# Kernel tuning notes

Measured on AMD Instinct MI355X. Metric: run time of the kernel, lower is better.

The kernel has to match this reference:

```python
import jax, jax.numpy as jnp
import numpy as np
from jax import lax


def _sobel_kernels3d(n1=1, n2=2, n3=2):
    Sx = np.asarray([[[-n1, 0, n1], [-n2, 0, n2], [-n1, 0, n1]],
                     [[-n2, 0, n2], [-n3 * n2, 0, n3 * n2], [-n2, 0, n2]],
                     [[-n1, 0, n1], [-n2, 0, n2], [-n1, 0, n1]]])
    Sy = np.asarray([[[-n1, -n2, -n1], [0, 0, 0], [n1, n2, n1]],
                     [[-n2, -n3 * n2, -n2], [0, 0, 0], [n2, n3 * n2, n2]],
                     [[-n1, -n2, -n1], [0, 0, 0], [n1, n2, n1]]])
    Sz = np.asarray([[[-n1, -n2, -n1], [-n2, -n3 * n2, -n2], [-n1, -n2, -n1]],
                     [[0, 0, 0], [0, 0, 0], [0, 0, 0]],
                     [[n1, n2, n1], [n2, n3 * n2, n2], [n1, n2, n1]]])
    Sd11 = np.asarray([[[0, n1, n2], [-n1, 0, n1], [-n2, -n1, 0]],
                       [[0, n2, n2 * n3], [-n2, 0, n2], [-n2 * n3, -n2, 0]],
                       [[0, n1, n2], [-n1, 0, n1], [-n2, -n1, 0]]])
    Sd12 = np.asarray([[[-n2, -n1, 0], [-n1, 0, n1], [0, n1, n2]],
                       [[-n2 * n3, -n2, 0], [-n2, 0, n2], [0, n2, n2 * n3]],
                       [[-n2, -n1, 0], [-n1, 0, n1], [0, n1, n2]]])
    Sd21 = Sd11.T
    Sd22 = Sd12.T
    Sd31 = np.asarray([-S.T for S in Sd11.T])
    Sd32 = np.asarray([S.T for S in Sd12.T])
    S = [Sx, Sy, Sz, Sd11, Sd12, Sd21, Sd22, Sd31, Sd32]
    # (9, 1, 3, 3, 3) OIDHW conv weight bank
    return np.stack(S).astype(np.float32)[:, None]


def _grad_edge3d(img, kernels, a=1):
    # img: (B, C, H, W, D); kernels: (9, 1, 3, 3, 3)
    B, C, H, W, D = img.shape
    p = jnp.pad(img, ((0, 0), (0, 0), (a, a), (a, a), (a, a)), mode='reflect')
    Hp, Wp, Dp = H + 2 * a, W + 2 * a, D + 2 * a
    # Each channel convolved independently with all 9 kernels in one conv call.
    xin = p.reshape(B * C, 1, Hp, Wp, Dp)
    conv = lax.conv_general_dilated(
        xin, kernels, window_strides=(1, 1, 1), padding='SAME',
        dimension_numbers=('NCDHW', 'OIDHW', 'NCDHW'))  # (B*C, 9, Hp, Wp, Dp)
    conv = conv.reshape(B, C, 9, Hp, Wp, Dp)
    # torch: sum_c (conv + 1e-6), squared per-filter, then sum_s (. + 1e-6), sqrt, * 1/C
    per_filter = jnp.sum(conv + 1e-6, axis=1)           # (B, 9, Hp, Wp, Dp)
    mag = jnp.sqrt(jnp.sum(per_filter ** 2, axis=1) + 9 * 1e-6) / C  # (B, Hp, Wp, Dp)
    mag = mag[:, a:-a, a:-a, a:-a]                      # (B, H, W, D)
    mn = mag.min()
    mx = mag.max()
    norm = (mag - mn) / (mx - mn + 1e-6)
    return norm.reshape(B, 1, H, W, D)


def setup_inputs() -> dict:
    key = jax.random.key(0)
    kx, ky = jax.random.split(key)
    B, C, H, W, D = 4, 1, 128, 128, 128
    x = jax.random.normal(kx, (B, C, H, W, D), dtype=jnp.float32)
    y = jax.random.normal(ky, (B, C, H, W, D), dtype=jnp.float32)
    kernels = jnp.asarray(_sobel_kernels3d(1, 2, 2))
    return {"x": x, "y": y, "kernels": kernels}


def reference(x, y, kernels):
    edge_x = _grad_edge3d(x, kernels)
    edge_y = _grad_edge3d(y, kernels)
    # lam_errors = [(1.0, L1Loss())], reduction='sum' -> 1e-6 + 1.0 * mean|ex-ey|
    l1 = jnp.mean(jnp.abs(edge_x - edge_y))
    return 1e-6 + 1.0 * l1
```

## Files before the change

kernel.cpp:

```cpp
#include <hip/hip_runtime.h>
#include <hip/hip_fp16.h>

#define HH 128
#define NB 4
#define NVOX (NB * HH * HH * HH)

#define NBLK1 2048
#define GRID2 512
#define TPB 256

typedef float vf2 __attribute__((ext_vector_type(2)));

__device__ __align__(16) unsigned int g_bmin[NBLK1];
__device__ __align__(16) unsigned int g_bmax[NBLK1];

union U4H8 { uint4 u; __half2 h[4]; };

__global__ __launch_bounds__(256) void pass1_kernel(
    const float* __restrict__ x, const float* __restrict__ y,
    __half* __restrict__ magx, __half* __restrict__ magy,
    float* __restrict__ out) {
    int bid = blockIdx.x;
    int tid = threadIdx.x;
    if (bid == 0 && tid == 0) out[0] = 0.0f;

    int lane = tid & 63, wid = tid >> 6;
    int wg  = bid & 15;
    int hs  = (bid >> 4) & 15;
    int b   = (bid >> 8) & 3;
    int img = bid >> 10;

    const float* __restrict__ src = img ? y : x;
    __half* __restrict__ dst = img ? magy : magx;

    int w0 = wg * 8 + wid * 2;
    int w1 = w0 + 1;
    int cw0 = (w0 == 0) ? 1 : (w0 - 1);
    int cw3 = (w1 == 127) ? 126 : (w1 + 1);
    int h0 = hs << 3;
    const vf2* base2 = (const vf2*)(src + ((size_t)b << 21));

    const vf2 two = {2.0f, 2.0f};
    const vf2 e1v = {1e-6f, 1e-6f};

    vf2 sbD[2][3], ubD[2][3], dbS[2][3], sbS[2][3], ubS[2][3], dbU[2][3], sbU[2][3];
    vf2 smn = {3.4e38f, 3.4e38f};
    vf2 smx = {0.0f, 0.0f};
    bool l0 = (lane == 0), l63 = (lane == 63);

    auto cstage = [&](vf2 q, vf2& S, vf2& D, vf2& U) {
        float Lxs = __shfl_up(q.y, 1);
        float Rys = __shfl_down(q.x, 1);
        float Lx = l0  ? q.y : Lxs;
        float Ry = l63 ? q.x : Rys;
        vf2 LV = {Lx, q.x};
        vf2 RV = {q.y, Ry};
        vf2 t = LV + RV;
        S = __builtin_elementwise_fma(two, q, t);
        D = RV - LV;
        U = t + q;
    };

#pragma unroll
    for (int r = 0; r < 10; ++r) {
        int hr = h0 + r - 1;
        hr = (hr < 0) ? 1 : ((hr > 127) ? 126 : hr);
        int rowb = (hr << 7);
        vf2 q0 = base2[(size_t)((rowb + cw0) << 6) + lane];
        vf2 q1 = base2[(size_t)((rowb + w0)  << 6) + lane];
        vf2 q2 = base2[(size_t)((rowb + w1)  << 6) + lane];
        vf2 q3 = base2[(size_t)((rowb + cw3) << 6) + lane];

        vf2 S[4], D[4], U[4];
        cstage(q0, S[0], D[0], U[0]);
        cstage(q1, S[1], D[1], U[1]);
        cstage(q2, S[2], D[2], U[2]);
        cstage(q3, S[3], D[3], U[3]);

        int slot = r % 3;
#pragma unroll
        for (int o = 0; o < 2; ++o) {
            vf2 D0 = D[o], D1 = D[o + 1], D2 = D[o + 2];
            vf2 S0 = S[o], S1 = S[o + 1], S2 = S[o + 2];
            vf2 U0 = U[o], U1 = U[o + 1], U2 = U[o + 2];
            vf2 tD = D0 + D2;
            sbD[o][slot] = __builtin_elementwise_fma(two, D1, tD);
            ubD[o][slot] = tD + D1;
            vf2 tS = S0 + S2;
            sbS[o][slot] = __builtin_elementwise_fma(two, S1, tS);
            ubS[o][slot] = tS + S1;
            dbS[o][slot] = S2 - S0;
            vf2 tU = U0 + U2;
            sbU[o][slot] = __builtin_elementwise_fma(two, U1, tU);
            dbU[o][slot] = U2 - U0;
        }

        if (r >= 2) {
            int s0 = (r - 2) % 3, s1 = (r - 1) % 3, s2 = slot;
            int hout = h0 + r - 2;
#pragma unroll
            for (int o = 0; o < 2; ++o) {
                vf2 tsbD = sbD[o][s0] + sbD[o][s2];
                vf2 Gssd = __builtin_elementwise_fma(two, sbD[o][s1], tsbD);
                vf2 Gusd = tsbD + sbD[o][s1];
                vf2 tubD = ubD[o][s0] + ubD[o][s2];
                vf2 Gsud = __builtin_elementwise_fma(two, ubD[o][s1], tubD);
                vf2 tdbS = dbS[o][s0] + dbS[o][s2];
                vf2 Gsds = __builtin_elementwise_fma(two, dbS[o][s1], tdbS);
                vf2 Guds = tdbS + dbS[o][s1];
                vf2 Gdss = sbS[o][s2] - sbS[o][s0];
                vf2 Gdus = ubS[o][s2] - ubS[o][s0];
                vf2 tdbU = dbU[o][s0] + dbU[o][s2];
                vf2 Gsdu = __builtin_elementwise_fma(two, dbU[o][s1], tdbU);
                vf2 Gdsu = sbU[o][s2] - sbU[o][s0];

                vf2 s1v = {9.0f * 1e-6f, 9.0f * 1e-6f};
                vf2 u;
                u = Gssd + e1v; s1v = __builtin_elementwise_fma(u, u, s1v);
                u = Gsds + e1v; s1v = __builtin_elementwise_fma(u, u, s1v);
                u = Gdss + e1v; s1v = __builtin_elementwise_fma(u, u, s1v);
                u = Gsud + e1v; vf2 s2v = u * u;
                s2v = __builtin_elementwise_fma(Gsdu, Gsdu, s2v);
                u = Gdus + e1v; s2v = __builtin_elementwise_fma(u, u, s2v);
                s2v = __builtin_elementwise_fma(Guds, Guds, s2v);
                u = Gusd + e1v; s2v = __builtin_elementwise_fma(u, u, s2v);
                s2v = __builtin_elementwise_fma(Gdsu, Gdsu, s2v);
                vf2 s = __builtin_elementwise_fma(two, s2v, s1v);

                smn = __builtin_elementwise_min(smn, s);
                smx = __builtin_elementwise_max(smx, s);

                float2 m2;
                m2.x = sqrtf(s.x);
                m2.y = sqrtf(s.y);
                __half2 hm2 = __float22half2_rn(m2);
                int h2idx = (((b * 128 + hout) * 128 + (w0 + o)) << 6) + lane;
                __builtin_nontemporal_store(*(unsigned int*)&hm2,
                    (unsigned int*)((__half2*)dst + h2idx));
            }
        }
    }

    unsigned int umn = __float_as_uint(fminf(smn.x, smn.y));
    unsigned int umx = __float_as_uint(fmaxf(smx.x, smx.y));
#pragma unroll
    for (int off = 32; off > 0; off >>= 1) {
        unsigned int a1 = __shfl_down(umn, off, 64);
        unsigned int b1 = __shfl_down(umx, off, 64);
        umn = (a1 < umn) ? a1 : umn;
        umx = (b1 > umx) ? b1 : umx;
    }
    __shared__ unsigned int smnsh[4], smxsh[4];
    if (lane == 0) { smnsh[wid] = umn; smxsh[wid] = umx; }
    __syncthreads();
    if (tid == 0) {
        unsigned int m0 = smnsh[0] < smnsh[1] ? smnsh[0] : smnsh[1];
        unsigned int m1 = smnsh[2] < smnsh[3] ? smnsh[2] : smnsh[3];
        unsigned int x0 = smxsh[0] > smxsh[1] ? smxsh[0] : smxsh[1];
        unsigned int x1 = smxsh[2] > smxsh[3] ? smxsh[2] : smxsh[3];
        float ms = __uint_as_float(m0 < m1 ? m0 : m1);
        float xs = __uint_as_float(x0 > x1 ? x0 : x1);
        float mnm = __half2float(__float2half_rn(sqrtf(ms)));
        float mxm = __half2float(__float2half_rn(sqrtf(xs)));
        g_bmin[bid] = __float_as_uint(mnm);
        g_bmax[bid] = __float_as_uint(mxm);
    }
}

__global__ __launch_bounds__(TPB) void pass2_kernel(
    const uint4* __restrict__ magx8, const uint4* __restrict__ magy8,
    float* __restrict__ out) {
    int tid = threadIdx.x, bid = blockIdx.x;
    int lane = tid & 63, wid = tid >> 6;
    __shared__ unsigned int sred[4][4];
    __shared__ float smm[4];
    __shared__ float sv[4];

    const uint4* bmin4 = (const uint4*)g_bmin;
    const uint4* bmax4 = (const uint4*)g_bmax;
    uint4 a = bmin4[tid];
    uint4 bq = bmax4[tid];
    uint4 c = bmin4[tid + 256];
    uint4 d = bmax4[tid + 256];
    unsigned int a01 = (a.x < a.y) ? a.x : a.y, a23 = (a.z < a.w) ? a.z : a.w;
    unsigned int b01 = (bq.x > bq.y) ? bq.x : bq.y, b23 = (bq.z > bq.w) ? bq.z : bq.w;
    unsigned int c01 = (c.x < c.y) ? c.x : c.y, c23 = (c.z < c.w) ? c.z : c.w;
    unsigned int d01 = (d.x > d.y) ? d.x : d.y, d23 = (d.z > d.w) ? d.z : d.w;
    unsigned int v0 = (a01 < a23) ? a01 : a23;
    unsigned int v1 = (b01 > b23) ? b01 : b23;
    unsigned int v2 = (c01 < c23) ? c01 : c23;
    unsigned int v3 = (d01 > d23) ? d01 : d23;
#pragma unroll
    for (int off = 32; off > 0; off >>= 1) {
        unsigned int t0 = __shfl_down(v0, off, 64);
        unsigned int t1 = __shfl_down(v1, off, 64);
        unsigned int t2 = __shfl_down(v2, off, 64);
        unsigned int t3 = __shfl_down(v3, off, 64);
        v0 = (t0 < v0) ? t0 : v0;
        v1 = (t1 > v1) ? t1 : v1;
        v2 = (t2 < v2) ? t2 : v2;
        v3 = (t3 > v3) ? t3 : v3;
    }
    if (lane == 0) { sred[wid][0] = v0; sred[wid][1] = v1; sred[wid][2] = v2; sred[wid][3] = v3; }
    __syncthreads();
    if (tid == 0) {
        unsigned int r0 = sred[0][0], r1 = sred[0][1], r2 = sred[0][2], r3 = sred[0][3];
#pragma unroll
        for (int w = 1; w < 4; ++w) {
            r0 = (sred[w][0] < r0) ? sred[w][0] : r0;
            r1 = (sred[w][1] > r1) ? sred[w][1] : r1;
            r2 = (sred[w][2] < r2) ? sred[w][2] : r2;
            r3 = (sred[w][3] > r3) ? sred[w][3] : r3;
        }
        smm[0] = __uint_as_float(r0);
        smm[1] = __uint_as_float(r1);
        smm[2] = __uint_as_float(r2);
        smm[3] = __uint_as_float(r3);
    }
    __syncthreads();

    float mnx = smm[0], mxx = smm[1], mny = smm[2], mxy = smm[3];
    float ix = 1.0f / (mxx - mnx + 1e-6f);
    float iy = 1.0f / (mxy - mny + 1e-6f);
    float cx = -mnx * ix;
    float cy = -mny * iy;

    float s = 0.0f;
#pragma unroll
    for (int k = 0; k < 8; ++k) {
        int i = bid * 2048 + k * TPB + tid;
        U4H8 qa, qb;
        qa.u = magx8[i];
        qb.u = magy8[i];
#pragma unroll
        for (int j = 0; j < 4; ++j) {
            float2 va = __half22float2(qa.h[j]);
            float2 vb = __half22float2(qb.h[j]);
            s += fabsf(fmaf(va.x, ix, cx) - fmaf(vb.x, iy, cy));
            s += fabsf(fmaf(va.y, ix, cx) - fmaf(vb.y, iy, cy));
        }
    }
#pragma unroll
    for (int off = 32; off > 0; off >>= 1) s += __shfl_down(s, off, 64);
    if (lane == 0) sv[wid] = s;
    __syncthreads();
    if (tid == 0) {
        float partial = ((sv[0] + sv[1]) + (sv[2] + sv[3])) * (1.0f / (float)NVOX);
        if (bid == 0) partial += 1e-6f;
        atomicAdd(out, partial);
    }
}

extern "C" void kernel_launch(void* const* d_in, const int* in_sizes, int n_in,
                              void* d_out, int out_size, void* d_ws, size_t ws_size,
                              hipStream_t stream) {
    const float* x = (const float*)d_in[0];
    const float* y = (const float*)d_in[1];
    float* out = (float*)d_out;

    __half* magx = (__half*)d_ws;
    __half* magy = magx + NVOX;

    pass1_kernel<<<NBLK1, 256, 0, stream>>>(x, y, magx, magy, out);
    pass2_kernel<<<GRID2, TPB, 0, stream>>>((const uint4*)magx, (const uint4*)magy, out);
}
```

Baseline: 132.9 us.

## Prefetch next row, drop epsilon adds, use raw hardware sqrt

The stencil loop now loads the next input row into registers before computing on the current one, so global load latency overlaps with arithmetic. The per-filter 1e-6 bias is dropped from each squared term. Precise sqrtf is replaced with the raw amdgcn sqrt intrinsic. Dropping the epsilon and using the approximate sqrt change numerics slightly, and the prefetch raises register pressure.

```diff
diff --git a/kernel.cpp b/kernel.cpp
--- a/kernel.cpp
+++ b/kernel.cpp
@@ -41,41 +41,47 @@
     const vf2* base2 = (const vf2*)(src + ((size_t)b << 21));
 
     const vf2 two = {2.0f, 2.0f};
-    const vf2 e1v = {1e-6f, 1e-6f};
 
     vf2 sbD[2][3], ubD[2][3], dbS[2][3], sbS[2][3], ubS[2][3], dbU[2][3], sbU[2][3];
     vf2 smn = {3.4e38f, 3.4e38f};
     vf2 smx = {0.0f, 0.0f};
     bool l0 = (lane == 0), l63 = (lane == 63);
 
-    auto cstage = [&](vf2 q, vf2& S, vf2& D, vf2& U) {
-        float Lxs = __shfl_up(q.y, 1);
-        float Rys = __shfl_down(q.x, 1);
-        float Lx = l0  ? q.y : Lxs;
-        float Ry = l63 ? q.x : Rys;
-        vf2 LV = {Lx, q.x};
-        vf2 RV = {q.y, Ry};
-        vf2 t = LV + RV;
-        S = __builtin_elementwise_fma(two, q, t);
-        D = RV - LV;
-        U = t + q;
-    };
-
-#pragma unroll
-    for (int r = 0; r < 10; ++r) {
+    auto loadrow = [&](int r, vf2* q) {
         int hr = h0 + r - 1;
         hr = (hr < 0) ? 1 : ((hr > 127) ? 126 : hr);
         int rowb = (hr << 7);
-        vf2 q0 = base2[(size_t)((rowb + cw0) << 6) + lane];
-        vf2 q1 = base2[(size_t)((rowb + w0)  << 6) + lane];
-        vf2 q2 = base2[(size_t)((rowb + w1)  << 6) + lane];
-        vf2 q3 = base2[(size_t)((rowb + cw3) << 6) + lane];
-
+        q[0] = base2[(size_t)((rowb + cw0) << 6) + lane];
+        q[1] = base2[(size_t)((rowb + w0)  << 6) + lane];
+        q[2] = base2[(size_t)((rowb + w1)  << 6) + lane];
+        q[3] = base2[(size_t)((rowb + cw3) << 6) + lane];
+    };
+
+    vf2 qc[4], qn[4];
+    loadrow(0, qc);
+
+#pragma unroll
+    for (int r = 0; r < 10; ++r) {
+        if (r < 9) loadrow(r + 1, qn);
+
+        float Lup[4], Rdn[4];
+#pragma unroll
+        for (int c = 0; c < 4; ++c) {
+            Lup[c] = __shfl_up(qc[c].y, 1);
+            Rdn[c] = __shfl_down(qc[c].x, 1);
+        }
         vf2 S[4], D[4], U[4];
-        cstage(q0, S[0], D[0], U[0]);
-        cstage(q1, S[1], D[1], U[1]);
-        cstage(q2, S[2], D[2], U[2]);
-        cstage(q3, S[3], D[3], U[3]);
+#pragma unroll
+        for (int c = 0; c < 4; ++c) {
+            float Lx = l0  ? qc[c].y : Lup[c];
+            float Ry = l63 ? qc[c].x : Rdn[c];
+            vf2 LV = {Lx, qc[c].x};
+            vf2 RV = {qc[c].y, Ry};
+            vf2 t = LV + RV;
+            S[c] = __builtin_elementwise_fma(two, qc[c], t);
+            D[c] = RV - LV;
+            U[c] = t + qc[c];
+        }
 
         int slot = r % 3;
 #pragma unroll
@@ -115,15 +121,14 @@
                 vf2 Gdsu = sbU[o][s2] - sbU[o][s0];
 
                 vf2 s1v = {9.0f * 1e-6f, 9.0f * 1e-6f};
-                vf2 u;
-                u = Gssd + e1v; s1v = __builtin_elementwise_fma(u, u, s1v);
-                u = Gsds + e1v; s1v = __builtin_elementwise_fma(u, u, s1v);
-                u = Gdss + e1v; s1v = __builtin_elementwise_fma(u, u, s1v);
-                u = Gsud + e1v; vf2 s2v = u * u;
+                s1v = __builtin_elementwise_fma(Gssd, Gssd, s1v);
+                s1v = __builtin_elementwise_fma(Gsds, Gsds, s1v);
+                s1v = __builtin_elementwise_fma(Gdss, Gdss, s1v);
+                vf2 s2v = Gsud * Gsud;
                 s2v = __builtin_elementwise_fma(Gsdu, Gsdu, s2v);
-                u = Gdus + e1v; s2v = __builtin_elementwise_fma(u, u, s2v);
+                s2v = __builtin_elementwise_fma(Gdus, Gdus, s2v);
                 s2v = __builtin_elementwise_fma(Guds, Guds, s2v);
-                u = Gusd + e1v; s2v = __builtin_elementwise_fma(u, u, s2v);
+                s2v = __builtin_elementwise_fma(Gusd, Gusd, s2v);
                 s2v = __builtin_elementwise_fma(Gdsu, Gdsu, s2v);
                 vf2 s = __builtin_elementwise_fma(two, s2v, s1v);
 
@@ -131,14 +136,17 @@
                 smx = __builtin_elementwise_max(smx, s);
 
                 float2 m2;
-                m2.x = sqrtf(s.x);
-                m2.y = sqrtf(s.y);
+                m2.x = __builtin_amdgcn_sqrtf(s.x);
+                m2.y = __builtin_amdgcn_sqrtf(s.y);
                 __half2 hm2 = __float22half2_rn(m2);
                 int h2idx = (((b * 128 + hout) * 128 + (w0 + o)) << 6) + lane;
                 __builtin_nontemporal_store(*(unsigned int*)&hm2,
                     (unsigned int*)((__half2*)dst + h2idx));
             }
         }
+
+#pragma unroll
+        for (int c = 0; c < 4; ++c) qc[c] = qn[c];
     }
 
     unsigned int umn = __float_as_uint(fminf(smn.x, smn.y));
@@ -160,8 +168,8 @@
         unsigned int x1 = smxsh[2] > smxsh[3] ? smxsh[2] : smxsh[3];
         float ms = __uint_as_float(m0 < m1 ? m0 : m1);
         float xs = __uint_as_float(x0 > x1 ? x0 : x1);
-        float mnm = __half2float(__float2half_rn(sqrtf(ms)));
-        float mxm = __half2float(__float2half_rn(sqrtf(xs)));
+        float mnm = __half2float(__float2half_rn(__builtin_amdgcn_sqrtf(ms)));
+        float mxm = __half2float(__float2half_rn(__builtin_amdgcn_sqrtf(xs)));
         g_bmin[bid] = __float_as_uint(mnm);
         g_bmax[bid] = __float_as_uint(mxm);
     }
```

Measured after the change: 127.7 us. 3.9% less time.
